# Optimization experiments

Measured on AMD Instinct MI355X. Metric: run time of the kernel, lower is better.

## Reference

```python
import jax, jax.numpy as jnp
import numpy as np

HEADS, DIM, N = 16, 128, 2048
NEG = -1e9


def setup_inputs() -> dict:
    key = jax.random.key(0)
    ks = jax.random.split(key, 8)
    xavier = lambda k, shape, fan: jax.random.uniform(
        k, shape, jnp.float32, -1.0, 1.0) * np.sqrt(6.0 / fan)
    return {
        "q": jax.random.normal(ks[0], (N, DIM), jnp.float32),
        "k": jax.random.normal(ks[1], (N, DIM), jnp.float32),
        "v": jax.random.normal(ks[2], (N, DIM), jnp.float32),
        "mask": jax.random.randint(ks[3], (N, N), 0, 2) > 0,
        "Q": xavier(ks[4], (HEADS, DIM, DIM), 2 * DIM),
        "K": xavier(ks[5], (HEADS, DIM, DIM), 2 * DIM),
        "V": xavier(ks[6], (HEADS, DIM, DIM), 2 * DIM),
        "last": xavier(ks[7], (HEADS * DIM, DIM), HEADS * DIM + DIM),
    }


def reference(q, k, v, Q, K, V, last, mask):
    # per-head projections: [n, d] x [h, d, d] -> [h, n, d]
    qp = jnp.einsum('nd,hde->hne', q, Q)
    kp = jnp.einsum('nd,hde->hne', k, K)
    vp = jnp.einsum('nd,hde->hne', v, V)
    n = qp.shape[1]
    # NOTE: original computes k @ q^T and scales by sqrt(seq_len) (q.size(1) after projection)
    att = jnp.einsum('hid,hjd->hij', kp, qp)  # [h, n, n]
    fmask = mask.astype(jnp.float32)
    att = att * fmask / jnp.sqrt(jnp.float32(n)) + NEG * (1.0 - fmask)
    att = jax.nn.softmax(att, axis=2)
    out = jnp.einsum('hij,hjd->hid', att, vp)            # [h, n, d]
    out = jnp.transpose(out, (1, 0, 2)).reshape(n, -1)   # n (heads d)
    return out @ last
```

## Files before the change

### kernel.cpp

```cpp
#include <hip/hip_runtime.h>
#include <hip/hip_bf16.h>


#define HN 16
#define NN 2048
#define DD 128

typedef __attribute__((ext_vector_type(8))) short short8;
typedef __attribute__((ext_vector_type(4))) short short4v;
typedef __attribute__((ext_vector_type(4))) float float4v;
typedef __attribute__((ext_vector_type(16))) float f32x16;
typedef __attribute__((ext_vector_type(4))) unsigned int uint4v;

#define CROW(r) ((((r) & 3)) + 8 * ((r) >> 2))

__device__ inline unsigned short f2bf(float f) {
    unsigned int u = __builtin_bit_cast(unsigned int, f);
    unsigned int r = (u + 0x7fffu + ((u >> 16) & 1u)) >> 16;
    return (unsigned short)r;
}

__device__ inline unsigned int cvtpk(float lo, float hi) {
    unsigned int w;
    asm("v_cvt_pk_bf16_f32 %0, %1, %2" : "=v"(w) : "v"(lo), "v"(hi));
    return w;
}

__device__ inline void plswap(unsigned int& x, unsigned int& y) {
#if __has_builtin(__builtin_amdgcn_permlane32_swap)
    typedef int int2v __attribute__((ext_vector_type(2)));
    int2v r = __builtin_amdgcn_permlane32_swap((int)x, (int)y, false, false);
    x = (unsigned int)r[0];
    y = (unsigned int)r[1];
#else
    const unsigned int sx = (unsigned int)__shfl_xor((int)x, 32);
    const unsigned int sy = (unsigned int)__shfl_xor((int)y, 32);
    const bool hiHalf = (threadIdx.x & 32) != 0;
    const unsigned int nx = hiHalf ? sy : x;
    const unsigned int ny = hiHalf ? y : sx;
    x = nx; y = ny;
#endif
}

__device__ inline short8 ld_bf8(const float* __restrict__ p) {
    const float4v a = *(const float4v*)p;
    const float4v b = *(const float4v*)(p + 4);
    short8 r;
    r[0] = (short)f2bf(a[0]); r[1] = (short)f2bf(a[1]);
    r[2] = (short)f2bf(a[2]); r[3] = (short)f2bf(a[3]);
    r[4] = (short)f2bf(b[0]); r[5] = (short)f2bf(b[1]);
    r[6] = (short)f2bf(b[2]); r[7] = (short)f2bf(b[3]);
    return r;
}

__device__ inline short8 ld2x4(const unsigned short* p) {
    const short4v lo = *(const short4v*)p;
    const short4v hi = *(const short4v*)(p + 4);
    short8 r;
    r[0] = lo[0]; r[1] = lo[1]; r[2] = lo[2]; r[3] = lo[3];
    r[4] = hi[0]; r[5] = hi[1]; r[6] = hi[2]; r[7] = hi[3];
    return r;
}

__global__ void sentinel_kernel(float* out, int n) {
    int i = blockIdx.x * 256 + threadIdx.x;
    if (i < n) out[i] = 2.0f;
}

__global__ __launch_bounds__(256) void zero_kernel(float* __restrict__ out, int n) {
    const int i4 = blockIdx.x * 256 + threadIdx.x;
    if (i4 * 4 + 3 < n) {
        *(float4v*)(out + i4 * 4) = float4v{0.f, 0.f, 0.f, 0.f};
    } else {
        for (int i = i4 * 4; i < n; i++) out[i] = 0.f;
    }
}

__global__ __launch_bounds__(256) void maskpack_kernel(
    const int* __restrict__ mask,
    unsigned long long* __restrict__ mb)
{
    const int word = blockIdx.x * 4 + (threadIdx.x >> 6);
    const int lane = threadIdx.x & 63;
    const int i = word >> 5;
    const int w = word & 31;
    const int mv = mask[(size_t)i * NN + w * 64 + lane];
    const unsigned long long b = __ballot(mv != 0);
    if (lane == 0) mb[word] = b;
}

__global__ __launch_bounds__(256) void proj_kernel(
    const float* __restrict__ q,
    const float* __restrict__ k,
    const float* __restrict__ v,
    const float* __restrict__ Qw,
    const float* __restrict__ Kw,
    const float* __restrict__ Vw,
    unsigned short* __restrict__ ws)
{
    __shared__ __align__(16) unsigned short Wt[128 * 132];
    const int t = blockIdx.z, h = blockIdx.y, rb = blockIdx.x;
    const int tid = threadIdx.x;
    const float* in = (t == 0) ? q : ((t == 1) ? k : v);
    const float* W  = ((t == 0) ? Qw : ((t == 1) ? Kw : Vw)) + h * DD * DD;
    unsigned short* out = ws + (size_t)t * (HN * NN * DD) + (size_t)h * (NN * DD);

    for (int idx2 = tid * 2; idx2 < DD * DD; idx2 += 512) {
        const int d = idx2 >> 7, e = idx2 & 127;
        const float2 w2 = *(const float2*)(W + idx2);
        Wt[(e + 0) * 132 + d] = f2bf(w2.x);
        Wt[(e + 1) * 132 + d] = f2bf(w2.y);
    }
    __syncthreads();

    const int wave = tid >> 6, lane = tid & 63;
    const int quad = lane >> 4, l16 = lane & 15;
    const int row0 = rb * 64 + wave * 16;

    float4v acc[8];
    for (int c = 0; c < 8; c++) acc[c] = {0.f, 0.f, 0.f, 0.f};

    if (t < 2) {
        for (int kk = 0; kk < 4; kk++) {
            const short8 a = ld_bf8(in + (size_t)(row0 + l16) * DD + kk * 32 + quad * 8);
            for (int c = 0; c < 8; c++) {
                const short8 b = ld2x4(&Wt[(c * 16 + l16) * 132 + kk * 32 + quad * 8]);
                acc[c] = __builtin_amdgcn_mfma_f32_16x16x32_bf16(a, b, acc[c], 0, 0, 0);
            }
        }
        for (int c = 0; c < 8; c++)
            for (int r = 0; r < 4; r++)
                out[(size_t)(row0 + quad * 4 + r) * DD + c * 16 + l16] = f2bf(acc[c][r]);
    } else {
        for (int kk = 0; kk < 4; kk++) {
            const short8 bv = ld_bf8(in + (size_t)(row0 + l16) * DD + kk * 32 + quad * 8);
            for (int c = 0; c < 8; c++) {
                const short8 aw = ld2x4(&Wt[(c * 16 + l16) * 132 + kk * 32 + quad * 8]);
                acc[c] = __builtin_amdgcn_mfma_f32_16x16x32_bf16(aw, bv, acc[c], 0, 0, 0);
            }
        }
        for (int c = 0; c < 8; c++)
            for (int r = 0; r < 4; r++)
                out[(size_t)(c * 16 + quad * 4 + r) * NN + row0 + l16] = f2bf(acc[c][r]);
    }
}

__global__ __launch_bounds__(256, 2) void attn_kernel(
    unsigned short* __restrict__ ws,
    const unsigned long long* __restrict__ mb)
{
    __shared__ __align__(16) unsigned short qs[2][64 * 136];
    __shared__ __align__(16) unsigned short vpTile[2][128 * 72];

    const int h = blockIdx.y, ib = blockIdx.x;
    const int tid = threadIdx.x;
    const int wave = tid >> 6, lane = tid & 63;
    const int ig = wave >> 1;
    const int h2 = wave & 1;
    const int l31 = lane & 31;
    const int hi = lane >> 5;

    const unsigned short* qp  = ws + (size_t)h * (NN * DD);
    const unsigned short* kp  = ws + (size_t)(HN * NN * DD) + (size_t)h * (NN * DD);
    const unsigned short* vpT = ws + (size_t)(2 * HN * NN * DD) + (size_t)h * (NN * DD);
    unsigned short* ao = ws + (size_t)(3 * HN * NN * DD);

    const int i0 = ib * 64;
    const float scale = 0.022097086912079612f;

    short8 kpf[8];
    {
        const int row = i0 + ig * 32 + l31;
#pragma unroll
        for (int kk = 0; kk < 8; kk++)
            kpf[kk] = *(const short8*)(kp + (size_t)row * DD + kk * 16 + hi * 8);
    }

    short8 rq[4], rv[4];

#define LOADT(J0) do {                                                         \
        _Pragma("unroll")                                                      \
        for (int it = 0; it < 4; it++) {                                       \
            const int idx = tid * 8 + it * 2048;                               \
            rq[it] = *(const short8*)(qp + (size_t)(J0) * DD + idx);           \
            rv[it] = *(const short8*)(vpT + (size_t)(idx >> 6) * NN + (J0) + (idx & 63)); \
        } } while (0)

#define WRITET(BUF) do {                                                       \
        _Pragma("unroll")                                                      \
        for (int it = 0; it < 4; it++) {                                       \
            const int idx = tid * 8 + it * 2048;                               \
            *(short8*)(&qs[BUF][(idx >> 7) * 136 + (idx & 127)]) = rq[it];     \
            *(short8*)(&vpTile[BUF][(idx >> 6) * 72 + (idx & 63)]) = rv[it];   \
        } } while (0)

    f32x16 o[4];
#pragma unroll
    for (int dt = 0; dt < 4; dt++)
#pragma unroll
        for (int r = 0; r < 16; r++) o[dt][r] = 0.f;
    float lacc = 0.f;

    auto COMPUTE = [&](int buf, int jt) {
        const unsigned long long mrow = mb[(size_t)(i0 + ig * 32 + l31) * 32 + jt];
        const unsigned int m2 = (unsigned int)(mrow >> (h2 * 32 + hi * 4));

        f32x16 s;
#pragma unroll
        for (int r = 0; r < 16; r++) s[r] = 0.f;
#pragma unroll
        for (int kk = 0; kk < 8; kk++) {
            const short8 aq = *(const short8*)(&qs[buf][(h2 * 32 + l31) * 136 + kk * 16 + hi * 8]);
            s = __builtin_amdgcn_mfma_f32_32x32x16_bf16(aq, kpf[kk], s, 0, 0, 0);
        }

#pragma unroll
        for (int r = 0; r < 16; r++) {
            const float x = ((m2 >> CROW(r)) & 1u) ? fmaf(s[r], scale, -5.0f) : -50.0f;
            s[r] = __expf(x);
        }
        float ls = (((s[0] + s[1]) + (s[2] + s[3])) + ((s[4] + s[5]) + (s[6] + s[7])))
                 + (((s[8] + s[9]) + (s[10] + s[11])) + ((s[12] + s[13]) + (s[14] + s[15])));
        ls += __shfl_xor(ls, 32);
        lacc += ls;

        short8 pa[2];
#pragma unroll
        for (int ks = 0; ks < 2; ks++) {
            const int b = ks * 8;
            unsigned int x0 = cvtpk(s[b + 0], s[b + 1]);
            unsigned int y0 = cvtpk(s[b + 4], s[b + 5]);
            unsigned int x1 = cvtpk(s[b + 2], s[b + 3]);
            unsigned int y1 = cvtpk(s[b + 6], s[b + 7]);
            plswap(x0, y0);
            plswap(x1, y1);
            uint4v w; w[0] = x0; w[1] = x1; w[2] = y0; w[3] = y1;
            pa[ks] = __builtin_bit_cast(short8, w);
        }

#pragma unroll
        for (int ks = 0; ks < 2; ks++) {
#pragma unroll
            for (int dt = 0; dt < 4; dt++) {
                const short8 bv = *(const short8*)(&vpTile[buf][(dt * 32 + l31) * 72 + h2 * 32 + ks * 16 + hi * 8]);
                o[dt] = __builtin_amdgcn_mfma_f32_32x32x16_bf16(pa[ks], bv, o[dt], 0, 0, 0);
            }
        }
    };

    LOADT(0);
    WRITET(0);
    LOADT(64);
    __syncthreads();

    int cur = 0;

#pragma unroll 1
    for (int jt = 0; jt < 30; ++jt) {
        WRITET(cur ^ 1);
        LOADT((jt + 2) * 64);
        COMPUTE(cur, jt);
        __syncthreads();
        cur ^= 1;
    }
    WRITET(cur ^ 1);
    COMPUTE(cur, 30);
    __syncthreads();
    cur ^= 1;
    COMPUTE(cur, 31);

#undef LOADT
#undef WRITET

    __syncthreads();
    float* obuf = (float*)&qs[0][0];
    float* lbuf = (float*)&vpTile[0][0];

    if (h2 == 1) {
#pragma unroll
        for (int dt = 0; dt < 4; dt++)
#pragma unroll
            for (int r = 0; r < 16; r++)
                obuf[(((ig * 2 + hi) * 4 + dt) * 16 + r) * 32 + l31] = o[dt][r];
        if (hi == 0) lbuf[ig * 32 + l31] = lacc;
    }
    __syncthreads();
    if (h2 == 0) {
        const float lt = lacc + lbuf[ig * 32 + l31];
        const float inv = (lt > 0.f) ? (1.0f / lt) : 0.f;
        if (hi == 0) lbuf[64 + ig * 32 + l31] = inv;
#pragma unroll
        for (int dt = 0; dt < 4; dt++)
#pragma unroll
            for (int r = 0; r < 16; r++) {
                const int row = CROW(r) + hi * 4;
                const float val = (o[dt][r] + obuf[(((ig * 2 + hi) * 4 + dt) * 16 + r) * 32 + l31])
                                  * lbuf[64 + ig * 32 + row];
                ao[(size_t)(i0 + ig * 32 + row) * (HN * DD) + h * DD + dt * 32 + l31] = f2bf(val);
            }
    }
}

__global__ __launch_bounds__(256) void final2_kernel(
    const unsigned short* __restrict__ ao,
    const float* __restrict__ last,
    float* __restrict__ outp)
{
    __shared__ __align__(16) unsigned short lt[32 * 516];
    const int tid = threadIdx.x;
    const int wave = tid >> 6, lane = tid & 63;
    const int quad = lane >> 4, l16 = lane & 15;
    const int i0 = blockIdx.x * 64;
    const int e0 = blockIdx.y * 32;
    const int k0 = blockIdx.z * 512;

#pragma unroll
    for (int idx2 = tid * 2; idx2 < 512 * 32; idx2 += 512) {
        const int kk = idx2 >> 5, e = idx2 & 31;
        const float2 w2 = *(const float2*)(last + (size_t)(k0 + kk) * DD + e0 + e);
        lt[(e + 0) * 516 + kk] = f2bf(w2.x);
        lt[(e + 1) * 516 + kk] = f2bf(w2.y);
    }
    __syncthreads();

    float4v acc[2];
    acc[0] = {0.f, 0.f, 0.f, 0.f};
    acc[1] = {0.f, 0.f, 0.f, 0.f};

    const unsigned short* arow = ao + (size_t)(i0 + wave * 16 + l16) * (HN * DD) + k0;

#pragma unroll
    for (int kb = 0; kb < 8; kb++) {
#pragma unroll
        for (int ks = 0; ks < 2; ks++) {
            const short8 a = *(const short8*)(arow + kb * 64 + ks * 32 + quad * 8);
#pragma unroll
            for (int dc = 0; dc < 2; dc++) {
                const short8 b = ld2x4(&lt[(dc * 16 + l16) * 516 + kb * 64 + ks * 32 + quad * 8]);
                acc[dc] = __builtin_amdgcn_mfma_f32_16x16x32_bf16(a, b, acc[dc], 0, 0, 0);
            }
        }
    }

#pragma unroll
    for (int r = 0; r < 4; r++)
#pragma unroll
        for (int dc = 0; dc < 2; dc++)
            atomicAdd(&outp[(size_t)(i0 + wave * 16 + quad * 4 + r) * DD + e0 + dc * 16 + l16],
                      acc[dc][r]);
}

extern "C" void kernel_launch(void* const* d_in, const int* in_sizes, int n_in,
                              void* d_out, int out_size, void* d_ws, size_t ws_size,
                              hipStream_t stream)
{
    const float* q    = (const float*)d_in[0];
    const float* k    = (const float*)d_in[1];
    const float* v    = (const float*)d_in[2];
    const int*   mask = (const int*)d_in[3];
    const float* Qw   = (const float*)d_in[4];
    const float* Kw   = (const float*)d_in[5];
    const float* Vw   = (const float*)d_in[6];
    const float* last = (const float*)d_in[7];
    unsigned short* ws  = (unsigned short*)d_ws;
    float* out = (float*)d_out;

    const size_t shorts_main = (size_t)4 * HN * NN * DD;
    const size_t mb_bytes = (size_t)NN * (NN / 64) * 8;
    const size_t needed = shorts_main * sizeof(unsigned short) + mb_bytes;
    if (ws_size < needed) {
        sentinel_kernel<<<(out_size + 255) / 256, 256, 0, stream>>>(out, out_size);
        return;
    }
    unsigned long long* mb = (unsigned long long*)(ws + shorts_main);

    zero_kernel<<<dim3((out_size / 4 + 255) / 256), 256, 0, stream>>>(out, out_size);
    maskpack_kernel<<<dim3(NN * (NN / 64) / 4), 256, 0, stream>>>(mask, mb);
    proj_kernel<<<dim3(32, 16, 3), 256, 0, stream>>>(q, k, v, Qw, Kw, Vw, ws);
    attn_kernel<<<dim3(32, 16), 256, 0, stream>>>(ws, mb);
    final2_kernel<<<dim3(32, 4, 4), 256, 0, stream>>>(ws + (size_t)3 * HN * NN * DD, last, out);
}
```

Measured before the change: 166.7 us.

## Load Q and V tiles directly from global into registers, dropping LDS staging

Replaces the LDS double-buffered staging of qp and vpT tiles (with block-wide barriers each iteration) by per-wave direct global loads into register fragments. Q fragments are double-buffered in registers across iterations and V fragments are loaded inside each compute step. This removes the LDS writes, reads and barriers, at the cost of redundant global/L2 traffic, since waves sharing the same j-tile each fetch it separately, plus higher register pressure. Exposed load latency is also a risk because V loads are issued right before use.

```diff
diff --git a/kernel.cpp b/kernel.cpp
--- a/kernel.cpp
+++ b/kernel.cpp
@@ -149,8 +149,8 @@
     unsigned short* __restrict__ ws,
     const unsigned long long* __restrict__ mb)
 {
-    __shared__ __align__(16) unsigned short qs[2][64 * 136];
-    __shared__ __align__(16) unsigned short vpTile[2][128 * 72];
+    __shared__ __align__(16) float obuf[8192];
+    __shared__ float lbuf[192];
 
     const int h = blockIdx.y, ib = blockIdx.x;
     const int tid = threadIdx.x;
@@ -176,24 +176,6 @@
             kpf[kk] = *(const short8*)(kp + (size_t)row * DD + kk * 16 + hi * 8);
     }
 
-    short8 rq[4], rv[4];
-
-#define LOADT(J0) do {                                                         \
-        _Pragma("unroll")                                                      \
-        for (int it = 0; it < 4; it++) {                                       \
-            const int idx = tid * 8 + it * 2048;                               \
-            rq[it] = *(const short8*)(qp + (size_t)(J0) * DD + idx);           \
-            rv[it] = *(const short8*)(vpT + (size_t)(idx >> 6) * NN + (J0) + (idx & 63)); \
-        } } while (0)
-
-#define WRITET(BUF) do {                                                       \
-        _Pragma("unroll")                                                      \
-        for (int it = 0; it < 4; it++) {                                       \
-            const int idx = tid * 8 + it * 2048;                               \
-            *(short8*)(&qs[BUF][(idx >> 7) * 136 + (idx & 127)]) = rq[it];     \
-            *(short8*)(&vpTile[BUF][(idx >> 6) * 72 + (idx & 63)]) = rv[it];   \
-        } } while (0)
-
     f32x16 o[4];
 #pragma unroll
     for (int dt = 0; dt < 4; dt++)
@@ -201,7 +183,25 @@
         for (int r = 0; r < 16; r++) o[dt][r] = 0.f;
     float lacc = 0.f;
 
-    auto COMPUTE = [&](int buf, int jt) {
+    short8 qfA[8], qfB[8];
+
+#define QLOAD(QF, J0) do {                                                      \
+        _Pragma("unroll")                                                       \
+        for (int kk = 0; kk < 8; kk++)                                          \
+            QF[kk] = *(const short8*)(qp + (size_t)((J0) + h2 * 32 + l31) * DD  \
+                                      + kk * 16 + hi * 8);                      \
+    } while (0)
+
+    auto COMPUTE = [&](const short8 (&qf)[8], int jt) {
+        short8 vf0[4], vf1[4];
+#pragma unroll
+        for (int dt = 0; dt < 4; dt++)
+            vf0[dt] = *(const short8*)(vpT + (size_t)(dt * 32 + l31) * NN
+                                       + jt * 64 + h2 * 32 + hi * 8);
+#pragma unroll
+        for (int dt = 0; dt < 4; dt++)
+            vf1[dt] = *(const short8*)(vpT + (size_t)(dt * 32 + l31) * NN
+                                       + jt * 64 + h2 * 32 + 16 + hi * 8);
         const unsigned long long mrow = mb[(size_t)(i0 + ig * 32 + l31) * 32 + jt];
         const unsigned int m2 = (unsigned int)(mrow >> (h2 * 32 + hi * 4));
 
@@ -209,10 +209,8 @@
 #pragma unroll
         for (int r = 0; r < 16; r++) s[r] = 0.f;
 #pragma unroll
-        for (int kk = 0; kk < 8; kk++) {
-            const short8 aq = *(const short8*)(&qs[buf][(h2 * 32 + l31) * 136 + kk * 16 + hi * 8]);
-            s = __builtin_amdgcn_mfma_f32_32x32x16_bf16(aq, kpf[kk], s, 0, 0, 0);
-        }
+        for (int kk = 0; kk < 8; kk++)
+            s = __builtin_amdgcn_mfma_f32_32x32x16_bf16(qf[kk], kpf[kk], s, 0, 0, 0);
 
 #pragma unroll
         for (int r = 0; r < 16; r++) {
@@ -239,42 +237,22 @@
         }
 
 #pragma unroll
-        for (int ks = 0; ks < 2; ks++) {
-#pragma unroll
-            for (int dt = 0; dt < 4; dt++) {
-                const short8 bv = *(const short8*)(&vpTile[buf][(dt * 32 + l31) * 72 + h2 * 32 + ks * 16 + hi * 8]);
-                o[dt] = __builtin_amdgcn_mfma_f32_32x32x16_bf16(pa[ks], bv, o[dt], 0, 0, 0);
-            }
-        }
+        for (int dt = 0; dt < 4; dt++)
+            o[dt] = __builtin_amdgcn_mfma_f32_32x32x16_bf16(pa[0], vf0[dt], o[dt], 0, 0, 0);
+#pragma unroll
+        for (int dt = 0; dt < 4; dt++)
+            o[dt] = __builtin_amdgcn_mfma_f32_32x32x16_bf16(pa[1], vf1[dt], o[dt], 0, 0, 0);
     };
 
-    LOADT(0);
-    WRITET(0);
-    LOADT(64);
-    __syncthreads();
-
-    int cur = 0;
-
+    QLOAD(qfA, 0);
 #pragma unroll 1
-    for (int jt = 0; jt < 30; ++jt) {
-        WRITET(cur ^ 1);
-        LOADT((jt + 2) * 64);
-        COMPUTE(cur, jt);
-        __syncthreads();
-        cur ^= 1;
-    }
-    WRITET(cur ^ 1);
-    COMPUTE(cur, 30);
-    __syncthreads();
-    cur ^= 1;
-    COMPUTE(cur, 31);
-
-#undef LOADT
-#undef WRITET
-
-    __syncthreads();
-    float* obuf = (float*)&qs[0][0];
-    float* lbuf = (float*)&vpTile[0][0];
+    for (int jt = 0; jt < 32; jt += 2) {
+        QLOAD(qfB, (jt + 1) * 64);
+        COMPUTE(qfA, jt);
+        QLOAD(qfA, (((jt + 2) & 31)) * 64);
+        COMPUTE(qfB, jt + 1);
+    }
+#undef QLOAD
 
     if (h2 == 1) {
 #pragma unroll
```

New measurement: 241.0 us. +44.6%, slower.
